# Optimization experiments

Hardware: AMD Instinct MI355X
Metric: run time of the kernel (lower is better)

## Reference

```python
import jax, jax.numpy as jnp
import numpy as np

N, G, E, H, OUT, MAX_N = 131072, 256, 384, 6, 256, 1024
DH = E // H  # 64


def _make_sizes():
    # variable-length segments summing exactly to N, each in [1, MAX_N]
    rng = np.random.default_rng(0)
    raw = rng.integers(128, 896, G).astype(np.int64)
    diff = int(N - raw.sum())
    q, r = divmod(diff, G)
    sizes = raw + q
    sizes[:r] += 1
    assert sizes.sum() == N and sizes.min() >= 1 and sizes.max() <= MAX_N
    return sizes


def setup_inputs() -> dict:
    key = jax.random.key(0)
    ks = jax.random.split(key, 8)
    s = 1.0 / np.sqrt(E)
    return {
        "node_feat": jax.random.normal(ks[0], (N, E), jnp.float32),
        "sizes": jnp.asarray(_make_sizes(), jnp.int32),
        "query": jax.random.normal(ks[1], (E,), jnp.float32),
        "Wq": jax.random.normal(ks[2], (E, E), jnp.float32) * s,
        "bq": jnp.zeros((E,), jnp.float32),
        "Wk": jax.random.normal(ks[3], (E, E), jnp.float32) * s,
        "bk": jnp.zeros((E,), jnp.float32),
        "Wv": jax.random.normal(ks[4], (E, E), jnp.float32) * s,
        "bv": jnp.zeros((E,), jnp.float32),
        "Wo": jax.random.normal(ks[5], (E, E), jnp.float32) * s,
        "bo": jnp.zeros((E,), jnp.float32),
        "Wp": jax.random.normal(ks[6], (OUT, E), jnp.float32) * s,
        "bp": jnp.zeros((OUT,), jnp.float32),
    }


def reference(node_feat, sizes, query, Wq, bq, Wk, bk, Wv, bv, Wo, bo, Wp, bp):
    # segment offsets and padded gather indices
    offsets = jnp.cumsum(sizes) - sizes                      # [G]
    pos = jnp.arange(MAX_N)
    idx = jnp.clip(offsets[:, None] + pos[None, :], 0, N - 1)  # [G, MAX_N]
    mask = pos[None, :] < sizes[:, None]                     # [G, MAX_N]

    # project K/V on the flat node table (one big GEMM), then gather into padded form
    k_flat = node_feat @ Wk.T + bk                           # [N, E]
    v_flat = node_feat @ Wv.T + bv
    k = k_flat[idx].reshape(G, MAX_N, H, DH)
    v = v_flat[idx].reshape(G, MAX_N, H, DH)

    # single shared query token, pre-scaled (PyTorch MHA scales q by 1/sqrt(head_dim))
    q = ((query @ Wq.T + bq) * (1.0 / np.sqrt(DH))).reshape(H, DH)

    scores = jnp.einsum('hd,gnhd->ghn', q, k)                # [G, H, MAX_N]
    scores = jnp.where(mask[:, None, :], scores, -1e30)
    attn = jax.nn.softmax(scores, axis=-1)
    pooled = jnp.einsum('ghn,gnhd->ghd', attn, v).reshape(G, E)

    out = pooled @ Wo.T + bo                                 # MHA out_proj
    return out @ Wp.T + bp                                   # final proj  [G, OUT]
```

## Files before the change

### kernel.cpp

```cpp
#include <hip/hip_runtime.h>
#include <math.h>

#define NN 131072
#define G  256
#define E  384
#define H  6
#define DH 64
#define OUTD 256
#define MAXN 1024

#define CHK 32
#define SLOTS 32
#define PART_STRIDE 2316

#define WS_QK   0
#define WS_C    2304
#define WS_OFF  2432
#define WS_QV   2944
#define WS_WL   3328
#define WS_M    11520
#define WS_CS   11776
#define WS_PART 12288
#define WS_WVT  (WS_PART + G*SLOTS*PART_STRIDE)
#define WS_WOT  (WS_WVT + E*E)
#define WS_WPT  (WS_WOT + E*E)

__global__ __launch_bounds__(256) void k0a_scan_qv(
    const int* __restrict__ sizes, const float* __restrict__ query,
    const float* __restrict__ Wq, const float* __restrict__ bq,
    float* __restrict__ wsf) {
  const int tid = threadIdx.x;
  if (blockIdx.x == 0) {
    __shared__ int s_scan[G];
    __shared__ int s_scan2[G];
    const int sz = sizes[tid];
    s_scan[tid] = sz;
    const int nch = (sz + CHK - 1) >> 5;
    s_scan2[tid] = nch;
    __syncthreads();
    for (int d = 1; d < G; d <<= 1) {
      int t = (tid >= d) ? s_scan[tid - d] : 0;
      int t2 = (tid >= d) ? s_scan2[tid - d] : 0;
      __syncthreads();
      s_scan[tid] += t;
      s_scan2[tid] += t2;
      __syncthreads();
    }
    ((int*)(wsf + WS_OFF))[tid] = s_scan[tid] - sz;
    const int pos = s_scan2[tid] - nch;
    ((int*)(wsf + WS_CS))[tid] = pos;
    int* wl = (int*)(wsf + WS_WL);
    for (int s = 0; s < nch; s++) wl[pos + s] = (tid << 5) | s;
    if (tid == G - 1) ((int*)(wsf + WS_M))[0] = s_scan2[G - 1];
  } else {
    const int lane = tid & 63;
    const int i = (blockIdx.x - 1) * 4 + (tid >> 6);
    float a = 0.f;
#pragma unroll
    for (int j = 0; j < 6; j++)
      a += Wq[(size_t)i * E + j * 64 + lane] * query[j * 64 + lane];
#pragma unroll
    for (int mm = 1; mm < 64; mm <<= 1) a += __shfl_xor(a, mm, 64);
    if (lane == 0) wsf[WS_QV + i] = 0.125f * (a + bq[i]);
  }
}

__global__ __launch_bounds__(256) void k0b_qk(
    const float* __restrict__ Wk, const float* __restrict__ bk,
    float* __restrict__ wsf) {
  __shared__ float qv_s[64];
  __shared__ float ps[256];
  const int h = blockIdx.x / 6, ec = blockIdx.x % 6;
  const int tid = threadIdx.x;
  if (tid < 64) qv_s[tid] = wsf[WS_QV + h * 64 + tid];
  __syncthreads();
  const int el = tid & 63, dq = tid >> 6;
  float a = 0.f;
#pragma unroll 4
  for (int d = dq * 16; d < dq * 16 + 16; d++)
    a += qv_s[d] * Wk[(size_t)(h * 64 + d) * E + ec * 64 + el];
  ps[tid] = a;
  __syncthreads();
  if (tid < 64)
    wsf[WS_QK + h * E + ec * 64 + tid] =
        ps[tid] + ps[64 + tid] + ps[128 + tid] + ps[192 + tid];
  if (ec == 0 && tid < 64) {
    float p = qv_s[tid] * bk[h * 64 + tid];
#pragma unroll
    for (int mm = 1; mm < 64; mm <<= 1) p += __shfl_xor(p, mm, 64);
    if (tid == 0) wsf[WS_C + h] = p;
  }
}

__global__ __launch_bounds__(256) void k0t_transpose(
    const float* __restrict__ Wv, const float* __restrict__ Wo,
    const float* __restrict__ Wp, float* __restrict__ wsf) {
  __shared__ float s[64][65];
  const int b = blockIdx.x;
  const float* src;
  float* dst;
  int R, tr, tc;
  if (b < 36)      { src = Wv; dst = wsf + WS_WVT; R = 384; tr = b / 6;        tc = b % 6; }
  else if (b < 72) { src = Wo; dst = wsf + WS_WOT; R = 384; tr = (b - 36) / 6; tc = (b - 36) % 6; }
  else             { src = Wp; dst = wsf + WS_WPT; R = 256; tr = (b - 72) / 6; tc = (b - 72) % 6; }
  const int r0 = tr * 64, c0 = tc * 64;
#pragma unroll
  for (int k = 0; k < 16; k++) {
    int idx = k * 256 + threadIdx.x;
    int r = idx >> 6, cc = idx & 63;
    s[r][cc] = src[(size_t)(r0 + r) * E + c0 + cc];
  }
  __syncthreads();
#pragma unroll
  for (int k = 0; k < 16; k++) {
    int idx = k * 256 + threadIdx.x;
    int cc = idx >> 6, r = idx & 63;
    dst[(size_t)(c0 + cc) * R + r0 + r] = s[r][cc];
  }
}

__global__ __launch_bounds__(128, 6) void k12_fused(
    const float* __restrict__ x, const int* __restrict__ sizes,
    float* __restrict__ wsf) {
  __shared__ float qk_l[8 * 292];
  __shared__ float c_s[8];
  __shared__ float pe[CHK * 8];
  const int M = ((const int*)(wsf + WS_M))[0];
  if ((int)blockIdx.x >= M) return;
  const int item = ((const int*)(wsf + WS_WL))[blockIdx.x];
  const int g = item >> 5, s = item & 31;
  const int Ng = sizes[g];
  const int rem = Ng - s * CHK;
  const int clen = rem < CHK ? rem : CHK;
  const int n0 = ((const int*)(wsf + WS_OFF))[g] + s * CHK;
  const int tid = threadIdx.x;
  const int lane = tid & 63, w = tid >> 6;

  for (int idx = tid; idx < 2304; idx += 128) {
    int sub = idx / 288, r3 = idx % 288;
    int h = r3 / 48, r2 = r3 % 48, j = r2 >> 2, r = r2 & 3;
    qk_l[sub * 292 + h * 48 + j * 4 + r] =
        wsf[WS_QK + h * E + (j * 8 + sub) * 4 + r];
  }
  if (tid < 8) c_s[tid] = (tid < 6) ? wsf[WS_C + tid] : 0.f;
  __syncthreads();

  const int sub = lane & 7, nod = lane >> 3;
  const float4* x4 = (const float4*)x;
  float* pslot = wsf + WS_PART + (size_t)blockIdx.x * PART_STRIDE;

  {
    float acc[2][6];
#pragma unroll
    for (int o = 0; o < 2; o++)
#pragma unroll
      for (int h = 0; h < 6; h++) acc[o][h] = 0.f;
#pragma unroll 4
    for (int j = 0; j < 12; j++) {
      float4 qk4[6];
#pragma unroll
      for (int h = 0; h < 6; h++)
        qk4[h] = *(const float4*)&qk_l[sub * 292 + h * 48 + j * 4];
      float4 xv[2];
#pragma unroll
      for (int o = 0; o < 2; o++) {
        int nn = w * 16 + o * 8 + nod;
        nn = nn < clen ? nn : clen - 1;
        xv[o] = x4[(size_t)(n0 + nn) * 96 + j * 8 + sub];
      }
#pragma unroll
      for (int o = 0; o < 2; o++)
#pragma unroll
        for (int h = 0; h < 6; h++)
          acc[o][h] += qk4[h].x * xv[o].x + qk4[h].y * xv[o].y
                     + qk4[h].z * xv[o].z + qk4[h].w * xv[o].w;
    }
#pragma unroll
    for (int o = 0; o < 2; o++) {
#pragma unroll
      for (int h = 0; h < 6; h++) {
        acc[o][h] += __shfl_xor(acc[o][h], 1, 64);
        acc[o][h] += __shfl_xor(acc[o][h], 2, 64);
        acc[o][h] += __shfl_xor(acc[o][h], 4, 64);
      }
      float v = acc[o][0];
#pragma unroll
      for (int h = 1; h < 6; h++) v = (sub == h) ? acc[o][h] : v;
      const int nl = w * 16 + o * 8 + nod;
      if (sub < 6)
        pe[nl * 8 + sub] = (nl < clen) ? v + c_s[sub] : -1.0e30f;
    }
  }
  __syncthreads();

  if (w == 0 && lane < 32) {
    const float4 sA = *(const float4*)&pe[lane * 8];
    const float2 sB = *(const float2*)&pe[lane * 8 + 4];
    float sc[6] = {sA.x, sA.y, sA.z, sA.w, sB.x, sB.y};
    float mh[6], lh[6], eh[6];
#pragma unroll
    for (int h = 0; h < 6; h++) {
      float t = sc[h];
#pragma unroll
      for (int mm = 1; mm < 32; mm <<= 1) t = fmaxf(t, __shfl_xor(t, mm, 32));
      mh[h] = t;
      eh[h] = __expf(sc[h] - t);
    }
#pragma unroll
    for (int h = 0; h < 6; h++) {
      float t = eh[h];
#pragma unroll
      for (int mm = 1; mm < 32; mm <<= 1) t += __shfl_xor(t, mm, 32);
      lh[h] = t;
    }
    *(float4*)&pe[lane * 8] = make_float4(eh[0], eh[1], eh[2], eh[3]);
    *(float2*)&pe[lane * 8 + 4] = make_float2(eh[4], eh[5]);
    if (lane < 6) {
      float vm = mh[0], vl = lh[0];
#pragma unroll
      for (int h = 1; h < 6; h++) {
        vm = (lane == h) ? mh[h] : vm;
        vl = (lane == h) ? lh[h] : vl;
      }
      pslot[2304 + lane] = vm;
      pslot[2310 + lane] = vl;
    }
  }
  __syncthreads();

  const float4* xr = x4 + (size_t)n0 * 96;
  if (w == 0) {
    float acc[6][4];
#pragma unroll
    for (int h = 0; h < 6; h++)
#pragma unroll
      for (int c = 0; c < 4; c++) acc[h][c] = 0.f;
#pragma unroll 2
    for (int n = 0; n < clen; n++) {
      const float4 xA = xr[n * 96 + lane];
      const float4 pA = *(const float4*)&pe[n * 8];
      const float2 pB = *(const float2*)&pe[n * 8 + 4];
      const float ph[6] = {pA.x, pA.y, pA.z, pA.w, pB.x, pB.y};
#pragma unroll
      for (int h = 0; h < 6; h++) {
        acc[h][0] += ph[h] * xA.x; acc[h][1] += ph[h] * xA.y;
        acc[h][2] += ph[h] * xA.z; acc[h][3] += ph[h] * xA.w;
      }
    }
#pragma unroll
    for (int h = 0; h < 6; h++)
      *(float4*)&pslot[h * E + lane * 4] =
          make_float4(acc[h][0], acc[h][1], acc[h][2], acc[h][3]);
  } else {
    float acc[6][4];
#pragma unroll
    for (int h = 0; h < 6; h++)
#pragma unroll
      for (int c = 0; c < 4; c++) acc[h][c] = 0.f;
    const int colB = 64 + (lane & 31);
    const int par = lane >> 5;
#pragma unroll 2
    for (int n = 0; n < CHK; n += 2) {
      const int nl = n + par;
      int nn = nl < clen ? nl : clen - 1;
      const float4 xB = xr[nn * 96 + colB];
      const float4 pA = *(const float4*)&pe[nl * 8];
      const float2 pB = *(const float2*)&pe[nl * 8 + 4];
      const float ph[6] = {pA.x, pA.y, pA.z, pA.w, pB.x, pB.y};
#pragma unroll
      for (int h = 0; h < 6; h++) {
        acc[h][0] += ph[h] * xB.x; acc[h][1] += ph[h] * xB.y;
        acc[h][2] += ph[h] * xB.z; acc[h][3] += ph[h] * xB.w;
      }
    }
#pragma unroll
    for (int h = 0; h < 6; h++)
#pragma unroll
      for (int c = 0; c < 4; c++)
        acc[h][c] += __shfl_xor(acc[h][c], 32, 64);
    if (lane < 32)
#pragma unroll
      for (int h = 0; h < 6; h++)
        *(float4*)&pslot[h * E + 256 + lane * 4] =
            make_float4(acc[h][0], acc[h][1], acc[h][2], acc[h][3]);
  }
}

__global__ __launch_bounds__(768) void k3_group(
    const float* __restrict__ wsf, const int* __restrict__ sizes,
    const float* __restrict__ bv, const float* __restrict__ bo,
    const float* __restrict__ bp, float* __restrict__ out) {
  __shared__ float xb[H * E];
  __shared__ float pooled[E];
  __shared__ float om[E];
  __shared__ float ps[768];
  __shared__ float msh[SLOTS][H], lsh[SLOTS][H], wgt[SLOTS][H];
  __shared__ float linv[H];
  const int tid = threadIdx.x;
  const int g = blockIdx.x;
  const int nch = (sizes[g] + CHK - 1) >> 5;
  const int base_s = ((const int*)(wsf + WS_CS))[g];
  const float* pg = wsf + WS_PART + (size_t)base_s * PART_STRIDE;
  const float* wvt = wsf + WS_WVT;
  const float* wot = wsf + WS_WOT;
  const float* wpt = wsf + WS_WPT;

  if (tid < SLOTS * H) {
    const int s2 = tid / H, h2 = tid % H;
    if (s2 < nch) {
      msh[s2][h2] = pg[(size_t)s2 * PART_STRIDE + 2304 + h2];
      lsh[s2][h2] = pg[(size_t)s2 * PART_STRIDE + 2310 + h2];
    }
  }
  __syncthreads();
  if (tid < H) {
    float m = -3.0e38f;
    for (int s = 0; s < nch; s++) m = fmaxf(m, msh[s][tid]);
    float L = 0.f;
    for (int s = 0; s < nch; s++) {
      float wv_ = __expf(msh[s][tid] - m);
      wgt[s][tid] = wv_;
      L += lsh[s][tid] * wv_;
    }
    linv[tid] = 1.f / L;
  }
  __syncthreads();
  for (int idx = tid; idx < H * E; idx += 768) {
    int h = idx / E;
    float a = 0.f;
    for (int s = 0; s < nch; s++) a += pg[(size_t)s * PART_STRIDE + idx] * wgt[s][h];
    xb[idx] = a * linv[h];
  }
  __syncthreads();

  {
    const int i = tid % 384, ks = tid / 384;
    const float* xh = xb + (i >> 6) * E + ks * 192;
    const float* wp_ = wvt + (size_t)(ks * 192) * E + i;
    float a0 = 0.f, a1 = 0.f, a2 = 0.f, a3 = 0.f;
#pragma unroll 4
    for (int e = 0; e < 192; e += 4) {
      a0 += wp_[(size_t)(e + 0) * E] * xh[e + 0];
      a1 += wp_[(size_t)(e + 1) * E] * xh[e + 1];
      a2 += wp_[(size_t)(e + 2) * E] * xh[e + 2];
      a3 += wp_[(size_t)(e + 3) * E] * xh[e + 3];
    }
    ps[tid] = (a0 + a1) + (a2 + a3);
  }
  __syncthreads();
  if (tid < 384) pooled[tid] = ps[tid] + ps[384 + tid] + bv[tid];
  __syncthreads();

  {
    const int i = tid % 384, ks = tid / 384;
    const float* xh = pooled + ks * 192;
    const float* wp_ = wot + (size_t)(ks * 192) * E + i;
    float a0 = 0.f, a1 = 0.f, a2 = 0.f, a3 = 0.f;
#pragma unroll 4
    for (int e = 0; e < 192; e += 4) {
      a0 += wp_[(size_t)(e + 0) * E] * xh[e + 0];
      a1 += wp_[(size_t)(e + 1) * E] * xh[e + 1];
      a2 += wp_[(size_t)(e + 2) * E] * xh[e + 2];
      a3 += wp_[(size_t)(e + 3) * E] * xh[e + 3];
    }
    ps[tid] = (a0 + a1) + (a2 + a3);
  }
  __syncthreads();
  if (tid < 384) om[tid] = ps[tid] + ps[384 + tid] + bo[tid];
  __syncthreads();

  {
    const int o = tid % 256, ks = tid / 256;
    const float* xh = om + ks * 128;
    const float* wp_ = wpt + (size_t)(ks * 128) * OUTD + o;
    float a0 = 0.f, a1 = 0.f, a2 = 0.f, a3 = 0.f;
#pragma unroll 4
    for (int e = 0; e < 128; e += 4) {
      a0 += wp_[(size_t)(e + 0) * OUTD] * xh[e + 0];
      a1 += wp_[(size_t)(e + 1) * OUTD] * xh[e + 1];
      a2 += wp_[(size_t)(e + 2) * OUTD] * xh[e + 2];
      a3 += wp_[(size_t)(e + 3) * OUTD] * xh[e + 3];
    }
    ps[tid] = (a0 + a1) + (a2 + a3);
  }
  __syncthreads();
  if (tid < 256)
    out[(size_t)g * OUTD + tid] = ps[tid] + ps[256 + tid] + ps[512 + tid] + bp[tid];
}

extern "C" void kernel_launch(void* const* d_in, const int* in_sizes, int n_in,
                              void* d_out, int out_size, void* d_ws, size_t ws_size,
                              hipStream_t stream) {
  const float* x     = (const float*)d_in[0];
  const int*   sizes = (const int*)d_in[1];
  const float* query = (const float*)d_in[2];
  const float* Wq    = (const float*)d_in[3];
  const float* bq    = (const float*)d_in[4];
  const float* Wk    = (const float*)d_in[5];
  const float* bk    = (const float*)d_in[6];
  const float* Wv    = (const float*)d_in[7];
  const float* bv    = (const float*)d_in[8];
  const float* Wo    = (const float*)d_in[9];
  const float* bo    = (const float*)d_in[10];
  const float* Wp    = (const float*)d_in[11];
  const float* bp    = (const float*)d_in[12];
  float* wsf = (float*)d_ws;
  float* out = (float*)d_out;

  hipLaunchKernelGGL(k0a_scan_qv, dim3(97), dim3(256), 0, stream,
                     sizes, query, Wq, bq, wsf);
  hipLaunchKernelGGL(k0b_qk, dim3(36), dim3(256), 0, stream, Wk, bk, wsf);
  hipLaunchKernelGGL(k0t_transpose, dim3(96), dim3(256), 0, stream,
                     Wv, Wo, Wp, wsf);
  hipLaunchKernelGGL(k12_fused, dim3(4352), dim3(128), 0, stream,
                     x, sizes, wsf);
  hipLaunchKernelGGL(k3_group, dim3(G), dim3(768), 0, stream,
                     wsf, sizes, bv, bo, bp, out);
}
```

Baseline: 366.4 us.

## Rewrite chunk kernel as one-wave-per-chunk online softmax with register-held query

Each 32-node chunk is now processed by a single wavefront that keeps the query-key vector in registers, computes the six head scores per node with a full-wave shuffle reduction, and folds them into a running online softmax and weighted accumulation. The shared-memory score buffer, the block barriers and the second read of x are removed, so each node row is read once. In exchange the per-node scores are computed serially, with six 64-lane shuffle reductions per node. The group kernel's partial combine is also unrolled by four with independent accumulators.

```diff
diff --git a/kernel.cpp b/kernel.cpp
--- a/kernel.cpp
+++ b/kernel.cpp
@@ -119,170 +119,113 @@
   }
 }
 
-__global__ __launch_bounds__(128, 6) void k12_fused(
+__global__ __launch_bounds__(256, 3) void k12_fused(
     const float* __restrict__ x, const int* __restrict__ sizes,
     float* __restrict__ wsf) {
-  __shared__ float qk_l[8 * 292];
-  __shared__ float c_s[8];
-  __shared__ float pe[CHK * 8];
   const int M = ((const int*)(wsf + WS_M))[0];
-  if ((int)blockIdx.x >= M) return;
-  const int item = ((const int*)(wsf + WS_WL))[blockIdx.x];
+  const int lane = threadIdx.x & 63;
+  const int it = blockIdx.x * 4 + (threadIdx.x >> 6);
+  if (it >= M) return;
+  const int item = ((const int*)(wsf + WS_WL))[it];
   const int g = item >> 5, s = item & 31;
-  const int Ng = sizes[g];
-  const int rem = Ng - s * CHK;
+  const int rem = sizes[g] - s * CHK;
   const int clen = rem < CHK ? rem : CHK;
   const int n0 = ((const int*)(wsf + WS_OFF))[g] + s * CHK;
-  const int tid = threadIdx.x;
-  const int lane = tid & 63, w = tid >> 6;
-
-  for (int idx = tid; idx < 2304; idx += 128) {
-    int sub = idx / 288, r3 = idx % 288;
-    int h = r3 / 48, r2 = r3 % 48, j = r2 >> 2, r = r2 & 3;
-    qk_l[sub * 292 + h * 48 + j * 4 + r] =
-        wsf[WS_QK + h * E + (j * 8 + sub) * 4 + r];
-  }
-  if (tid < 8) c_s[tid] = (tid < 6) ? wsf[WS_C + tid] : 0.f;
-  __syncthreads();
-
-  const int sub = lane & 7, nod = lane >> 3;
-  const float4* x4 = (const float4*)x;
-  float* pslot = wsf + WS_PART + (size_t)blockIdx.x * PART_STRIDE;
-
-  {
-    float acc[2][6];
-#pragma unroll
-    for (int o = 0; o < 2; o++)
-#pragma unroll
-      for (int h = 0; h < 6; h++) acc[o][h] = 0.f;
-#pragma unroll 4
-    for (int j = 0; j < 12; j++) {
-      float4 qk4[6];
-#pragma unroll
-      for (int h = 0; h < 6; h++)
-        qk4[h] = *(const float4*)&qk_l[sub * 292 + h * 48 + j * 4];
-      float4 xv[2];
-#pragma unroll
-      for (int o = 0; o < 2; o++) {
-        int nn = w * 16 + o * 8 + nod;
-        nn = nn < clen ? nn : clen - 1;
-        xv[o] = x4[(size_t)(n0 + nn) * 96 + j * 8 + sub];
+
+  float qk[6][6], cb[6];
+#pragma unroll
+  for (int h = 0; h < 6; h++) {
+#pragma unroll
+    for (int k = 0; k < 6; k++) qk[h][k] = wsf[WS_QK + h * E + k * 64 + lane];
+    cb[h] = wsf[WS_C + h];
+  }
+
+  float m[6], l[6], acc[6][6];
+#pragma unroll
+  for (int h = 0; h < 6; h++) {
+    m[h] = -3.0e38f;
+    l[h] = 0.f;
+#pragma unroll
+    for (int k = 0; k < 6; k++) acc[h][k] = 0.f;
+  }
+
+  const float* xp = x + (size_t)n0 * E + lane;
+
+  float xA[6], xB[6];
+  auto loadx = [&](float (&b)[6], int n) {
+    const float* p = xp + n * E;
+#pragma unroll
+    for (int k = 0; k < 6; k++) b[k] = p[k * 64];
+  };
+  auto compute = [&](const float (&xv)[6]) {
+    float sr[6];
+#pragma unroll
+    for (int h = 0; h < 6; h++) {
+      float a = qk[h][0] * xv[0];
+#pragma unroll
+      for (int k = 1; k < 6; k++) a = fmaf(qk[h][k], xv[k], a);
+#pragma unroll
+      for (int mm = 1; mm < 64; mm <<= 1) a += __shfl_xor(a, mm, 64);
+      sr[h] = a + cb[h];
+    }
+    bool upd = false;
+#pragma unroll
+    for (int h = 0; h < 6; h++) upd = upd || (sr[h] > m[h]);
+    if (upd) {
+#pragma unroll
+      for (int h = 0; h < 6; h++) {
+        const float nm = fmaxf(m[h], sr[h]);
+        const float f = __expf(m[h] - nm);
+        m[h] = nm;
+        l[h] *= f;
+#pragma unroll
+        for (int k = 0; k < 6; k++) acc[h][k] *= f;
       }
-#pragma unroll
-      for (int o = 0; o < 2; o++)
-#pragma unroll
-        for (int h = 0; h < 6; h++)
-          acc[o][h] += qk4[h].x * xv[o].x + qk4[h].y * xv[o].y
-                     + qk4[h].z * xv[o].z + qk4[h].w * xv[o].w;
-    }
-#pragma unroll
-    for (int o = 0; o < 2; o++) {
-#pragma unroll
-      for (int h = 0; h < 6; h++) {
-        acc[o][h] += __shfl_xor(acc[o][h], 1, 64);
-        acc[o][h] += __shfl_xor(acc[o][h], 2, 64);
-        acc[o][h] += __shfl_xor(acc[o][h], 4, 64);
+    }
+#pragma unroll
+    for (int h = 0; h < 6; h++) {
+      const float p = __expf(sr[h] - m[h]);
+      l[h] += p;
+#pragma unroll
+      for (int k = 0; k < 6; k++) acc[h][k] = fmaf(p, xv[k], acc[h][k]);
+    }
+  };
+
+  loadx(xA, 0);
+  int n = 0;
+  while (true) {
+    if (n + 1 < clen) {
+      loadx(xB, n + 1);
+      compute(xA);
+      if (n + 2 < clen) {
+        loadx(xA, n + 2);
+        compute(xB);
+        n += 2;
+      } else {
+        compute(xB);
+        break;
       }
-      float v = acc[o][0];
-#pragma unroll
-      for (int h = 1; h < 6; h++) v = (sub == h) ? acc[o][h] : v;
-      const int nl = w * 16 + o * 8 + nod;
-      if (sub < 6)
-        pe[nl * 8 + sub] = (nl < clen) ? v + c_s[sub] : -1.0e30f;
-    }
-  }
-  __syncthreads();
-
-  if (w == 0 && lane < 32) {
-    const float4 sA = *(const float4*)&pe[lane * 8];
-    const float2 sB = *(const float2*)&pe[lane * 8 + 4];
-    float sc[6] = {sA.x, sA.y, sA.z, sA.w, sB.x, sB.y};
-    float mh[6], lh[6], eh[6];
-#pragma unroll
-    for (int h = 0; h < 6; h++) {
-      float t = sc[h];
-#pragma unroll
-      for (int mm = 1; mm < 32; mm <<= 1) t = fmaxf(t, __shfl_xor(t, mm, 32));
-      mh[h] = t;
-      eh[h] = __expf(sc[h] - t);
-    }
-#pragma unroll
-    for (int h = 0; h < 6; h++) {
-      float t = eh[h];
-#pragma unroll
-      for (int mm = 1; mm < 32; mm <<= 1) t += __shfl_xor(t, mm, 32);
-      lh[h] = t;
-    }
-    *(float4*)&pe[lane * 8] = make_float4(eh[0], eh[1], eh[2], eh[3]);
-    *(float2*)&pe[lane * 8 + 4] = make_float2(eh[4], eh[5]);
-    if (lane < 6) {
-      float vm = mh[0], vl = lh[0];
-#pragma unroll
-      for (int h = 1; h < 6; h++) {
-        vm = (lane == h) ? mh[h] : vm;
-        vl = (lane == h) ? lh[h] : vl;
-      }
-      pslot[2304 + lane] = vm;
-      pslot[2310 + lane] = vl;
-    }
-  }
-  __syncthreads();
-
-  const float4* xr = x4 + (size_t)n0 * 96;
-  if (w == 0) {
-    float acc[6][4];
-#pragma unroll
-    for (int h = 0; h < 6; h++)
-#pragma unroll
-      for (int c = 0; c < 4; c++) acc[h][c] = 0.f;
-#pragma unroll 2
-    for (int n = 0; n < clen; n++) {
-      const float4 xA = xr[n * 96 + lane];
-      const float4 pA = *(const float4*)&pe[n * 8];
-      const float2 pB = *(const float2*)&pe[n * 8 + 4];
-      const float ph[6] = {pA.x, pA.y, pA.z, pA.w, pB.x, pB.y};
-#pragma unroll
-      for (int h = 0; h < 6; h++) {
-        acc[h][0] += ph[h] * xA.x; acc[h][1] += ph[h] * xA.y;
-        acc[h][2] += ph[h] * xA.z; acc[h][3] += ph[h] * xA.w;
-      }
-    }
-#pragma unroll
-    for (int h = 0; h < 6; h++)
-      *(float4*)&pslot[h * E + lane * 4] =
-          make_float4(acc[h][0], acc[h][1], acc[h][2], acc[h][3]);
-  } else {
-    float acc[6][4];
-#pragma unroll
-    for (int h = 0; h < 6; h++)
-#pragma unroll
-      for (int c = 0; c < 4; c++) acc[h][c] = 0.f;
-    const int colB = 64 + (lane & 31);
-    const int par = lane >> 5;
-#pragma unroll 2
-    for (int n = 0; n < CHK; n += 2) {
-      const int nl = n + par;
-      int nn = nl < clen ? nl : clen - 1;
-      const float4 xB = xr[nn * 96 + colB];
-      const float4 pA = *(const float4*)&pe[nl * 8];
-      const float2 pB = *(const float2*)&pe[nl * 8 + 4];
-      const float ph[6] = {pA.x, pA.y, pA.z, pA.w, pB.x, pB.y};
-#pragma unroll
-      for (int h = 0; h < 6; h++) {
-        acc[h][0] += ph[h] * xB.x; acc[h][1] += ph[h] * xB.y;
-        acc[h][2] += ph[h] * xB.z; acc[h][3] += ph[h] * xB.w;
-      }
-    }
-#pragma unroll
-    for (int h = 0; h < 6; h++)
-#pragma unroll
-      for (int c = 0; c < 4; c++)
-        acc[h][c] += __shfl_xor(acc[h][c], 32, 64);
-    if (lane < 32)
-#pragma unroll
-      for (int h = 0; h < 6; h++)
-        *(float4*)&pslot[h * E + 256 + lane * 4] =
-            make_float4(acc[h][0], acc[h][1], acc[h][2], acc[h][3]);
+    } else {
+      compute(xA);
+      break;
+    }
+  }
+
+  float* pslot = wsf + WS_PART + (size_t)it * PART_STRIDE;
+#pragma unroll
+  for (int h = 0; h < 6; h++)
+#pragma unroll
+    for (int k = 0; k < 6; k++)
+      pslot[h * E + k * 64 + lane] = acc[h][k];
+  if (lane < 6) {
+    float vm = m[0], vl = l[0];
+#pragma unroll
+    for (int h = 1; h < 6; h++) {
+      vm = (lane == h) ? m[h] : vm;
+      vl = (lane == h) ? l[h] : vl;
+    }
+    pslot[2304 + lane] = vm;
+    pslot[2310 + lane] = vl;
   }
 }
 
@@ -326,10 +269,18 @@
   }
   __syncthreads();
   for (int idx = tid; idx < H * E; idx += 768) {
-    int h = idx / E;
-    float a = 0.f;
-    for (int s = 0; s < nch; s++) a += pg[(size_t)s * PART_STRIDE + idx] * wgt[s][h];
-    xb[idx] = a * linv[h];
+    const int h = idx / E;
+    const float* pp = pg + idx;
+    float a0 = 0.f, a1 = 0.f, a2 = 0.f, a3 = 0.f;
+    int s2 = 0;
+    for (; s2 + 3 < nch; s2 += 4) {
+      a0 += pp[(size_t)(s2 + 0) * PART_STRIDE] * wgt[s2 + 0][h];
+      a1 += pp[(size_t)(s2 + 1) * PART_STRIDE] * wgt[s2 + 1][h];
+      a2 += pp[(size_t)(s2 + 2) * PART_STRIDE] * wgt[s2 + 2][h];
+      a3 += pp[(size_t)(s2 + 3) * PART_STRIDE] * wgt[s2 + 3][h];
+    }
+    for (; s2 < nch; s2++) a0 += pp[(size_t)s2 * PART_STRIDE] * wgt[s2][h];
+    xb[idx] = ((a0 + a1) + (a2 + a3)) * linv[h];
   }
   __syncthreads();
 
@@ -412,7 +363,7 @@
   hipLaunchKernelGGL(k0b_qk, dim3(36), dim3(256), 0, stream, Wk, bk, wsf);
   hipLaunchKernelGGL(k0t_transpose, dim3(96), dim3(256), 0, stream,
                      Wv, Wo, Wp, wsf);
-  hipLaunchKernelGGL(k12_fused, dim3(4352), dim3(128), 0, stream,
+  hipLaunchKernelGGL(k12_fused, dim3(1088), dim3(256), 0, stream,
                      x, sizes, wsf);
   hipLaunchKernelGGL(k3_group, dim3(G), dim3(768), 0, stream,
                      wsf, sizes, bv, bo, bp, out);
```

Result: slower. 560.6 us (+53.0%).
